# Kernel tuning notes

Hardware: AMD Instinct MI355X
Metric: run time of the kernel (lower is better)

The kernel has to match this reference:

```python
import jax, jax.numpy as jnp
import numpy as np

FEATURE_SCALE = 0.25  # cfg.feature_scale
G = 4                 # deformable/offset groups
K = 3                 # deform kernel size
KK = K * K
PAD = 1


def conv2d(x, w, b=None):
    y = jax.lax.conv_general_dilated(x, w, (1, 1), ((PAD, PAD), (PAD, PAD)),
                                     dimension_numbers=('NCHW', 'OIHW', 'NCHW'))
    return y if b is None else y + b[None, :, None, None]


def bilinear_upsample_ac(x, fs):
    # F.interpolate(mode='bilinear', align_corners=True, scale_factor=fs)
    b, c, H, W = x.shape
    Ho, Wo = H * fs, W * fs
    sy = jnp.arange(Ho, dtype=x.dtype) * ((H - 1) / (Ho - 1))
    sx = jnp.arange(Wo, dtype=x.dtype) * ((W - 1) / (Wo - 1))
    y0 = jnp.clip(jnp.floor(sy).astype(jnp.int32), 0, H - 2)
    x0 = jnp.clip(jnp.floor(sx).astype(jnp.int32), 0, W - 2)
    wy = (sy - y0)[None, None, :, None]
    wx = (sx - x0)[None, None, None, :]
    rows = x[:, :, y0, :] * (1 - wy) + x[:, :, y0 + 1, :] * wy
    return rows[:, :, :, x0] * (1 - wx) + rows[:, :, :, x0 + 1] * wx


def deform_conv(x, offset, mask, w):
    # torchvision.ops.deform_conv2d, stride 1, pad 1, weight groups = 1,
    # offset/mask groups = G. offset layout: (b, G*KK*2, H, W), (dy, dx) pairs.
    b, C, H, W = x.shape
    Cg = C // G
    off = offset.reshape(b, G, KK, 2, H, W)
    ii = (jnp.arange(KK) // K).reshape(1, 1, KK, 1, 1).astype(x.dtype)
    jj = (jnp.arange(KK) % K).reshape(1, 1, KK, 1, 1).astype(x.dtype)
    ys = jnp.arange(H, dtype=x.dtype).reshape(1, 1, 1, H, 1)
    xs = jnp.arange(W, dtype=x.dtype).reshape(1, 1, 1, 1, W)
    py = ys - PAD + ii + off[:, :, :, 0]   # (b,G,KK,H,W)
    px = xs - PAD + jj + off[:, :, :, 1]
    xt = x.reshape(b, G, Cg, H, W).transpose(0, 1, 3, 4, 2)  # (b,G,H,W,Cg)
    y0f = jnp.floor(py)
    x0f = jnp.floor(px)
    wy = py - y0f
    wx = px - x0f
    y0 = y0f.astype(jnp.int32)
    x0 = x0f.astype(jnp.int32)
    bi = jnp.arange(b).reshape(b, 1, 1, 1, 1)
    gi = jnp.arange(G).reshape(1, G, 1, 1, 1)

    def corner(yi, xi, wgt):
        valid = ((yi >= 0) & (yi < H) & (xi >= 0) & (xi < W)).astype(x.dtype)
        v = xt[bi, gi, jnp.clip(yi, 0, H - 1), jnp.clip(xi, 0, W - 1)]  # (b,G,KK,H,W,Cg)
        return v * (wgt * valid)[..., None]

    s = (corner(y0, x0, (1 - wy) * (1 - wx)) + corner(y0, x0 + 1, (1 - wy) * wx)
         + corner(y0 + 1, x0, wy * (1 - wx)) + corner(y0 + 1, x0 + 1, wy * wx))
    s = s * mask.reshape(b, G, KK, H, W)[..., None]
    wr = w.reshape(w.shape[0], G, Cg, KK)
    return jnp.einsum('bgkhwc,ogck->bohw', s, wr)


def _align(sou_list, ref_list, params):
    cat_feat, offset_vs = [], []
    for i in (3, 2, 1):
        sou, ref = sou_list[i - 1], ref_list[i - 1]
        b, C, H, W = sou.shape
        Cg = C // G
        off_w, off_b, mod_w, mod_b, reg_w = params[i]
        off_in = jnp.concatenate([sou.reshape(b, G, Cg, H, W),
                                  ref.reshape(b, G, Cg, H, W)], axis=2)
        off_in = off_in.reshape(b * G, 2 * Cg, H, W)
        offset = conv2d(off_in, off_w, off_b).reshape(b, G * 2 * KK, H, W)
        rng = min(H, W) * 0.5 / 2
        offset_map = rng * 2 * jax.nn.sigmoid(offset) - rng
        modulator = 2.0 * jax.nn.sigmoid(conv2d(sou, mod_w, mod_b))
        feat = deform_conv(sou, offset_map, modulator, reg_w)
        fs = int(1 // (FEATURE_SCALE / 2 ** (i - 1)))
        oy = jnp.mean(offset_map[:, 0::2], axis=1, keepdims=True)
        ox = jnp.mean(offset_map[:, 1::2], axis=1, keepdims=True)
        ov = bilinear_upsample_ac(jnp.concatenate([oy, ox], axis=1), fs) * fs
        cat_feat.append(feat)
        offset_vs.append(ov)
    return tuple(cat_feat) + tuple(offset_vs)


def setup_inputs() -> dict:
    key = jax.random.key(0)
    ks = jax.random.split(key, 32)
    d = {}
    shapes = {1: (2, 64, 128, 128), 2: (2, 64, 64, 64), 3: (2, 64, 32, 32)}
    k = 0
    for i in (1, 2, 3):
        d[f'sou{i}'] = jax.random.normal(ks[k], shapes[i], jnp.float32); k += 1
        d[f'ref{i}'] = jax.random.normal(ks[k], shapes[i], jnp.float32); k += 1
    Cg = 64 // G
    for i in (1, 2, 3):
        d[f'off_w{i}'] = jax.random.normal(ks[k], (2 * KK, 2 * Cg, K, K), jnp.float32) * 0.05; k += 1
        d[f'off_b{i}'] = jax.random.normal(ks[k], (2 * KK,), jnp.float32) * 0.05; k += 1
        d[f'mod_w{i}'] = jax.random.normal(ks[k], (G * KK, 64, K, K), jnp.float32) * 0.05; k += 1
        d[f'mod_b{i}'] = jax.random.normal(ks[k], (G * KK,), jnp.float32) * 0.05; k += 1
        d[f'reg_w{i}'] = jax.random.normal(ks[k], (64, 64, K, K), jnp.float32) * 0.05; k += 1
    return d


def reference(sou1, sou2, sou3, ref1, ref2, ref3,
              off_w1, off_b1, mod_w1, mod_b1, reg_w1,
              off_w2, off_b2, mod_w2, mod_b2, reg_w2,
              off_w3, off_b3, mod_w3, mod_b3, reg_w3):
    params = {1: (off_w1, off_b1, mod_w1, mod_b1, reg_w1),
              2: (off_w2, off_b2, mod_w2, mod_b2, reg_w2),
              3: (off_w3, off_b3, mod_w3, mod_b3, reg_w3)}
    return _align([sou1, sou2, sou3], [ref1, ref2, ref3], params)
```

## Files before the change

kernel.cpp:

```cpp
#include <hip/hip_runtime.h>

typedef __attribute__((ext_vector_type(8))) short short8;
typedef __attribute__((ext_vector_type(4))) float f32x4;

__device__ __forceinline__ float sigmoidf_(float x) { return 1.f / (1.f + __expf(-x)); }
__device__ __forceinline__ unsigned bf16rne(float x) {
    unsigned b = __float_as_uint(x);
    return (b + 0x7FFFu + ((b >> 16) & 1u)) >> 16;
}


struct P {
    const float *sou0, *sou1, *sou2;
    const float *ref0, *ref1, *ref2;
    const float *ob0, *ob1, *ob2;
    const float *mb0, *mb1, *mb2;
    float* out;
    float* ws;
};

union U {
    uint4 u4; int4 i4; short8 s8; f32x4 f4;
};

__global__ __launch_bounds__(256) void repack_all(
    const float* __restrict__ ow0, const float* __restrict__ mw0, const float* __restrict__ rw0,
    const float* __restrict__ ow1, const float* __restrict__ mw1, const float* __restrict__ rw1,
    const float* __restrict__ ow2, const float* __restrict__ mw2, const float* __restrict__ rw2,
    float* __restrict__ dst) {
    const int lvl = blockIdx.y;
    const float* ow = lvl == 0 ? ow0 : (lvl == 1 ? ow1 : ow2);
    const float* mw = lvl == 0 ? mw0 : (lvl == 1 ? mw1 : mw2);
    const float* rw = lvl == 0 ? rw0 : (lvl == 1 ? rw1 : rw2);
    unsigned* d = (unsigned*)(dst + lvl * 62784);
    int i = blockIdx.x * 256 + threadIdx.x;
    if (i < 18432) {
        int jw = i & 3;
        int lane = (i >> 2) & 63;
        int t3 = i >> 8;
        int ks = t3 % 18, wvu = t3 / 18;
        int o = wvu * 16 + (lane & 15);
        int c0 = ks * 32 + (lane >> 4) * 8 + 2 * jw;
        int g0 = c0 / 144, r0 = c0 % 144;
        int c1 = c0 + 1;
        int g1 = c1 / 144, r1 = c1 % 144;
        float w0 = rw[o * 576 + (g0 * 16 + (r0 & 15)) * 9 + (r0 >> 4)];
        float w1 = rw[o * 576 + (g1 * 16 + (r1 & 15)) * 9 + (r1 >> 4)];
        d[i] = bf16rne(w0) | (bf16rne(w1) << 16);
    } else if (i < 23552) {
        int o2 = i - 18432;
        int jw = o2 & 3;
        int lane = (o2 >> 2) & 63;
        int t2 = o2 >> 8;
        int nt = t2 & 1;
        int hk = t2 >> 1;
        int ks = hk % 5, h = hk / 5;
        int n = nt * 16 + (lane & 15);
        int K = ks * 32 + (lane >> 4) * 8 + 2 * jw;
        int tap = K >> 4, ch = K & 15;
        bool ok = (n < 18) && (tap < 9);
        float w0 = ok ? ow[n * 288 + (h * 16 + ch) * 9 + tap] : 0.f;
        float w1 = ok ? ow[n * 288 + (h * 16 + ch + 1) * 9 + tap] : 0.f;
        d[36864 + o2] = bf16rne(w0) | (bf16rne(w1) << 16);
    } else if (i < 37376) {
        int o3 = i - 23552;
        int jw = o3 & 3;
        int lane = (o3 >> 2) & 63;
        int t3 = o3 >> 8;
        int nt = t3 % 3, tc = t3 / 3;
        int tap = tc >> 1, c = tc & 1;
        int n = nt * 16 + (lane & 15);
        int ic0 = c * 32 + (lane >> 4) * 8 + 2 * jw;
        float w0 = (n < 36) ? mw[n * 576 + ic0 * 9 + tap] : 0.f;
        float w1 = (n < 36) ? mw[n * 576 + (ic0 + 1) * 9 + tap] : 0.f;
        d[41984 + o3] = bf16rne(w0) | (bf16rne(w1) << 16);
    }
}

__global__ __launch_bounds__(256, 2) void k1_prep(P p) {
    __shared__ __align__(16) char smem[28512];
    const int t = blockIdx.x;
    float* ws = p.ws;
    const int tid = threadIdx.x;

    int lvl, j;
    if (t < 512) { lvl = 0; j = t; }
    else if (t < 640) { lvl = 1; j = t - 512; }
    else { lvl = 2; j = t - 640; }
    const int logW = 7 - lvl;
    const int W = 1 << logW, H = W, HW = H * W;
    const int nper = 256 >> (2 * lvl);
    const int qb = j % nper, b = j / nper;
    const int q0 = qb * 64;
    const int hlo = q0 >> logW;
    const int xlo = q0 & (W - 1);
    const int cols = (W >= 64) ? 66 : 34;
    const int rcTot = (W >= 64) ? 198 : 136;
    const float* sou = lvl == 0 ? p.sou0 : (lvl == 1 ? p.sou1 : p.sou2);
    const float* ref = lvl == 0 ? p.ref0 : (lvl == 1 ? p.ref1 : p.ref2);
    const float* base_s = sou + (size_t)b * 64 * HW;
    const float* base_r = ref + (size_t)b * 64 * HW;
    unsigned* ldsW = (unsigned*)smem;
    const bool sact = tid < rcTot;
    const int srow = tid / cols, scol = tid - srow * cols;
    const int grow = hlo - 1 + srow, gcol = xlo - 1 + scol;
    const bool inb = sact && grow >= 0 && grow < H && gcol >= 0 && gcol < W;
    const size_t goff = inb ? ((size_t)grow * W + gcol) : 0;

    float vs[64];
#pragma unroll
    for (int c8 = 0; c8 < 8; ++c8) {
        const float* p0 = base_s + (size_t)(c8 * 8) * HW;
#pragma unroll
        for (int jj = 0; jj < 8; ++jj)
            vs[c8 * 8 + jj] = inb ? p0[(size_t)jj * HW + goff] : 0.f;
    }
    if (sact) {
#pragma unroll
        for (int c8 = 0; c8 < 8; ++c8) {
            uint4 wv;
            wv.x = bf16rne(vs[c8 * 8 + 0]) | (bf16rne(vs[c8 * 8 + 1]) << 16);
            wv.y = bf16rne(vs[c8 * 8 + 2]) | (bf16rne(vs[c8 * 8 + 3]) << 16);
            wv.z = bf16rne(vs[c8 * 8 + 4]) | (bf16rne(vs[c8 * 8 + 5]) << 16);
            wv.w = bf16rne(vs[c8 * 8 + 6]) | (bf16rne(vs[c8 * 8 + 7]) << 16);
            *(uint4*)&ldsW[tid * 36 + c8 * 4] = wv;
        }
    }
    __syncthreads();

    unsigned* XTb = (unsigned*)(ws + 4919232) +
                    (lvl == 0 ? 0 : (lvl == 1 ? 1048576 : 1310720));
#pragma unroll
    for (int u = 0; u < 2; ++u) {
        const int idx = tid * 2 + u;
        const int px = idx >> 3, gh = idx & 7;
        const int g = gh >> 1, half = gh & 1;
        const int rc = ((px >> logW) + 1) * cols + (px & (W - 1)) + 1;
        uint4 vv = *(const uint4*)&ldsW[rc * 36 + g * 8 + half * 4];
        *(uint4*)(XTb + ((size_t)(b * 4 + g) * HW + q0 + px) * 8 + half * 4) = vv;
    }

    float vr[64];
#pragma unroll
    for (int c8 = 0; c8 < 8; ++c8) {
        const float* p0 = base_r + (size_t)(c8 * 8) * HW;
#pragma unroll
        for (int jj = 0; jj < 8; ++jj)
            vr[c8 * 8 + jj] = inb ? p0[(size_t)jj * HW + goff] : 0.f;
    }

    const int wvu = __builtin_amdgcn_readfirstlane(tid >> 6);
    const int lane = tid & 63, quad = lane >> 4, lo16 = lane & 15;
    const int qg = q0 + wvu * 16 + lo16;
    const int rowB = (qg >> logW) - hlo;
    const int colB = (qg & (W - 1)) - xlo;
    const unsigned short* ldsS = (const unsigned short*)smem;
    const unsigned* WREPu = (const unsigned*)(ws + 4730880 + lvl * 62784);
    const unsigned* WBO2 = WREPu + 36864;
    const unsigned* WBM = WREPu + 41984;

    f32x4 accM[3], accO[4][2];
#pragma unroll
    for (int nt = 0; nt < 3; ++nt) accM[nt] = (f32x4){0.f, 0.f, 0.f, 0.f};
#pragma unroll
    for (int g = 0; g < 4; ++g)
#pragma unroll
        for (int nt = 0; nt < 2; ++nt) accO[g][nt] = (f32x4){0.f, 0.f, 0.f, 0.f};

#pragma unroll
    for (int tap = 0; tap < 9; ++tap) {
        const int ky = tap / 3, kx = tap - ky * 3;
        const int rc = (rowB + ky) * cols + colB + kx;
#pragma unroll
        for (int c = 0; c < 2; ++c) {
            U au; au.s8 = *(const short8*)&ldsS[rc * 72 + c * 32 + quad * 8];
#pragma unroll
            for (int nt = 0; nt < 3; ++nt) {
                U bu;
                bu.u4 = *(const uint4*)(WBM + (((tap * 2 + c) * 3 + nt) * 64 + lane) * 4);
                accM[nt] = __builtin_amdgcn_mfma_f32_16x16x32_bf16(au.s8, bu.s8, accM[nt], 0, 0, 0);
            }
        }
    }
#pragma unroll
    for (int ks = 0; ks < 5; ++ks) {
        const int Kbase = ks * 32 + quad * 8;
        const int tap = min(Kbase >> 4, 8);
        const int ky = tap / 3, kx = tap - ky * 3;
        const int rc = (rowB + ky) * cols + colB + kx;
        const int choff = Kbase & 15;
        U bu0, bu1;
        bu0.u4 = *(const uint4*)(WBO2 + ((ks * 2 + 0) * 64 + lane) * 4);
        bu1.u4 = *(const uint4*)(WBO2 + ((ks * 2 + 1) * 64 + lane) * 4);
#pragma unroll
        for (int g = 0; g < 4; ++g) {
            U au; au.s8 = *(const short8*)&ldsS[rc * 72 + g * 16 + choff];
            accO[g][0] = __builtin_amdgcn_mfma_f32_16x16x32_bf16(au.s8, bu0.s8, accO[g][0], 0, 0, 0);
            accO[g][1] = __builtin_amdgcn_mfma_f32_16x16x32_bf16(au.s8, bu1.s8, accO[g][1], 0, 0, 0);
        }
    }
    __syncthreads();

    if (sact) {
#pragma unroll
        for (int c8 = 0; c8 < 8; ++c8) {
            uint4 wv;
            wv.x = bf16rne(vr[c8 * 8 + 0]) | (bf16rne(vr[c8 * 8 + 1]) << 16);
            wv.y = bf16rne(vr[c8 * 8 + 2]) | (bf16rne(vr[c8 * 8 + 3]) << 16);
            wv.z = bf16rne(vr[c8 * 8 + 4]) | (bf16rne(vr[c8 * 8 + 5]) << 16);
            wv.w = bf16rne(vr[c8 * 8 + 6]) | (bf16rne(vr[c8 * 8 + 7]) << 16);
            *(uint4*)&ldsW[tid * 36 + c8 * 4] = wv;
        }
    }
    __syncthreads();

#pragma unroll
    for (int ks = 0; ks < 5; ++ks) {
        const int Kbase = ks * 32 + quad * 8;
        const int tap = min(Kbase >> 4, 8);
        const int ky = tap / 3, kx = tap - ky * 3;
        const int rc = (rowB + ky) * cols + colB + kx;
        const int choff = Kbase & 15;
        U bu0, bu1;
        bu0.u4 = *(const uint4*)(WBO2 + (((5 + ks) * 2 + 0) * 64 + lane) * 4);
        bu1.u4 = *(const uint4*)(WBO2 + (((5 + ks) * 2 + 1) * 64 + lane) * 4);
#pragma unroll
        for (int g = 0; g < 4; ++g) {
            U au; au.s8 = *(const short8*)&ldsS[rc * 72 + g * 16 + choff];
            accO[g][0] = __builtin_amdgcn_mfma_f32_16x16x32_bf16(au.s8, bu0.s8, accO[g][0], 0, 0, 0);
            accO[g][1] = __builtin_amdgcn_mfma_f32_16x16x32_bf16(au.s8, bu1.s8, accO[g][1], 0, 0, 0);
        }
    }

    {
        const float* bias = lvl == 0 ? p.mb0 : (lvl == 1 ? p.mb1 : p.mb2);
        float* MOD = ws + (lvl == 0 ? 3096576 : (lvl == 1 ? 4276224 : 4571136));
#pragma unroll
        for (int nt = 0; nt < 3; ++nt) {
            const int o = nt * 16 + lo16;
            if (o < 36) {
                const float bb = bias[o];
                float* op = MOD + (size_t)(b * 36 + o) * HW + q0 + wvu * 16 + quad * 4;
                *(float4*)op = make_float4(2.f * sigmoidf_(accM[nt][0] + bb),
                                           2.f * sigmoidf_(accM[nt][1] + bb),
                                           2.f * sigmoidf_(accM[nt][2] + bb),
                                           2.f * sigmoidf_(accM[nt][3] + bb));
            }
        }
    }
    {
        const float* bias = lvl == 0 ? p.ob0 : (lvl == 1 ? p.ob1 : p.ob2);
        float* OFFM = ws + (lvl == 0 ? 0 : (lvl == 1 ? 2359296 : 2949120));
        const float rng = 0.25f * (float)H;
        float macc[4] = {0.f, 0.f, 0.f, 0.f};
#pragma unroll
        for (int g = 0; g < 4; ++g)
#pragma unroll
            for (int nt = 0; nt < 2; ++nt) {
                const int o = nt * 16 + lo16;
                if (o < 18) {
                    const float bb = bias[o];
                    float ovv[4];
#pragma unroll
                    for (int rg = 0; rg < 4; ++rg)
                        ovv[rg] = rng * (2.f * sigmoidf_(accO[g][nt][rg] + bb) - 1.f);
                    float* op = OFFM + (size_t)(b * 72 + g * 18 + o) * HW + q0 + wvu * 16 + quad * 4;
                    *(float4*)op = make_float4(ovv[0], ovv[1], ovv[2], ovv[3]);
#pragma unroll
                    for (int rg = 0; rg < 4; ++rg) macc[rg] += ovv[rg];
                }
            }
        const bool odd = (lo16 & 1) != 0;
        float my[4], mx[4];
#pragma unroll
        for (int rg = 0; rg < 4; ++rg) {
            my[rg] = odd ? 0.f : macc[rg];
            mx[rg] = odd ? macc[rg] : 0.f;
        }
#pragma unroll
        for (int m = 1; m < 16; m <<= 1) {
#pragma unroll
            for (int rg = 0; rg < 4; ++rg) {
                my[rg] += __shfl_xor(my[rg], m);
                mx[rg] += __shfl_xor(mx[rg], m);
            }
        }
        if (lo16 == 0) {
            float* MEAN = ws + (lvl == 0 ? 4644864 : (lvl == 1 ? 4710400 : 4726784));
            const int pxb = q0 + wvu * 16 + quad * 4;
            const float inv = 1.f / 36.f;
            *(float4*)(MEAN + (size_t)(b * 2) * HW + pxb) =
                make_float4(my[0] * inv, my[1] * inv, my[2] * inv, my[3] * inv);
            *(float4*)(MEAN + (size_t)(b * 2 + 1) * HW + pxb) =
                make_float4(mx[0] * inv, mx[1] * inv, mx[2] * inv, mx[3] * inv);
        }
    }
}

__global__ __launch_bounds__(256) void k2_fused(P p) {
    __shared__ __align__(16) unsigned lds[32 * 292];
    const int t = blockIdx.x;
    float* ws = p.ws;
    const int tid = threadIdx.x;
    if (t < 1344) {
        int lvl, j;
        if (t < 1024) { lvl = 0; j = t; }
        else if (t < 1280) { lvl = 1; j = t - 1024; }
        else { lvl = 2; j = t - 1280; }
        const int logW = 7 - lvl;
        const int W = 1 << logW, H = W, HW = H * W;
        const int nper = 512 >> (2 * lvl);
        const int qb = j % nper, b = j / nper;
        const int q0 = qb * 32;
        const float* OFFM = ws + (lvl == 0 ? 0 : (lvl == 1 ? 2359296 : 2949120));
        const float* MOD = ws + (lvl == 0 ? 3096576 : (lvl == 1 ? 4276224 : 4571136));
        const unsigned* XTb = (const unsigned*)(ws + 4919232) +
                              (lvl == 0 ? 0 : (lvl == 1 ? 1048576 : 1310720));
        const unsigned* WB = (const unsigned*)(ws + 4730880 + lvl * 62784);
        float* outp = p.out + (lvl == 0 ? 655360 : (lvl == 1 ? 131072 : 0));
        const int wvu = __builtin_amdgcn_readfirstlane(tid >> 6);
        const int lane = tid & 63, quad = lane >> 4, lo16 = lane & 15;

        float dyv[5], dxv[5], mmv[5];
#pragma unroll
        for (int it = 0; it < 5; ++it) {
            const int tsk = it * 256 + tid;
            if (tsk < 1152) {
                const int gk = tsk >> 5, px = tsk & 31;
                const int g = gk / 9, k = gk - g * 9;
                const int q = q0 + px;
                dyv[it] = OFFM[(size_t)(b * 72 + g * 18 + 2 * k) * HW + q];
                dxv[it] = OFFM[(size_t)(b * 72 + g * 18 + 2 * k + 1) * HW + q];
                mmv[it] = MOD[(size_t)(b * 36 + g * 9 + k) * HW + q];
            }
        }
#pragma unroll
        for (int it = 0; it < 5; ++it) {
            const int tsk = it * 256 + tid;
            if (tsk < 1152) {
                const int gk = tsk >> 5, px = tsk & 31;
                const int g = gk / 9, k = gk - g * 9;
                const int q = q0 + px;
                const int h = q >> logW, xp = q & (W - 1);
                const int ky = k / 3, kx = k - ky * 3;
                float py = (float)(h - 1 + ky) + dyv[it];
                float pxx = (float)(xp - 1 + kx) + dxv[it];
                float y0f = floorf(py), x0f = floorf(pxx);
                float wy = py - y0f, wx = pxx - x0f;
                int y0 = (int)y0f, x0 = (int)x0f;
                const unsigned* xg = XTb + (size_t)(b * 4 + g) * HW * 8;
                float s[16];
#pragma unroll
                for (int cc = 0; cc < 16; ++cc) s[cc] = 0.f;
#pragma unroll
                for (int cor = 0; cor < 4; ++cor) {
                    int yy = y0 + (cor >> 1), xx = x0 + (cor & 1);
                    float cw = ((cor >> 1) ? wy : 1.f - wy) * ((cor & 1) ? wx : 1.f - wx);
                    cw = (yy >= 0 && yy < H && xx >= 0 && xx < W) ? cw * mmv[it] : 0.f;
                    int yc = min(max(yy, 0), H - 1), xc = min(max(xx, 0), W - 1);
                    const uint4* cp = (const uint4*)(xg + (size_t)((yc << logW) + xc) * 8);
                    unsigned cbuf[8];
                    *(uint4*)&cbuf[0] = cp[0];
                    *(uint4*)&cbuf[4] = cp[1];
#pragma unroll
                    for (int pr = 0; pr < 8; ++pr) {
                        float lo = __uint_as_float(cbuf[pr] << 16);
                        float hi = __uint_as_float(cbuf[pr] & 0xFFFF0000u);
                        s[2 * pr] = fmaf(cw, lo, s[2 * pr]);
                        s[2 * pr + 1] = fmaf(cw, hi, s[2 * pr + 1]);
                    }
                }
                unsigned* dp = &lds[px * 292 + gk * 8];
                uint4 w0, w1;
                w0.x = bf16rne(s[0]) | (bf16rne(s[1]) << 16);
                w0.y = bf16rne(s[2]) | (bf16rne(s[3]) << 16);
                w0.z = bf16rne(s[4]) | (bf16rne(s[5]) << 16);
                w0.w = bf16rne(s[6]) | (bf16rne(s[7]) << 16);
                w1.x = bf16rne(s[8]) | (bf16rne(s[9]) << 16);
                w1.y = bf16rne(s[10]) | (bf16rne(s[11]) << 16);
                w1.z = bf16rne(s[12]) | (bf16rne(s[13]) << 16);
                w1.w = bf16rne(s[14]) | (bf16rne(s[15]) << 16);
                *(uint4*)dp = w0;
                *(uint4*)(dp + 4) = w1;
            }
        }
        __syncthreads();

        f32x4 acc[2];
        acc[0] = (f32x4){0.f, 0.f, 0.f, 0.f};
        acc[1] = (f32x4){0.f, 0.f, 0.f, 0.f};
#pragma unroll
        for (int ks = 0; ks < 18; ++ks) {
            U bu;
            bu.u4 = *(const uint4*)(WB + (((wvu * 18 + ks) * 64 + lane) << 2));
#pragma unroll
            for (int mt = 0; mt < 2; ++mt) {
                U au;
                au.u4 = *(const uint4*)&lds[(mt * 16 + lo16) * 292 + ks * 16 + quad * 4];
                acc[mt] = __builtin_amdgcn_mfma_f32_16x16x32_bf16(au.s8, bu.s8, acc[mt], 0, 0, 0);
            }
        }
        float* op = outp + (size_t)(b * 64 + wvu * 16 + lo16) * HW + q0;
#pragma unroll
        for (int mt = 0; mt < 2; ++mt)
            *(f32x4*)(op + mt * 16 + quad * 4) = acc[mt];
    } else {
        int flat = ((t - 1344) * 256 + tid) * 4;
        int lvl = flat >> 20;
        int r = flat & 1048575;
        int b = r >> 19, c = (r >> 18) & 1;
        int pix = r & 262143;
        int yo = pix >> 9, xo = pix & 511;
        const int H = 128 >> lvl, W = H;
        const float* MEAN = ws + (lvl == 0 ? 4644864 : (lvl == 1 ? 4710400 : 4726784));
        const float* m = MEAN + (size_t)(b * 2 + c) * H * W;
        float* o = p.out + (lvl == 0 ? 4849664 : (lvl == 1 ? 3801088 : 2752512)) +
                   ((size_t)(b * 2 + c) * 512 + yo) * 512 + xo;
        const float fs = (float)(4 << lvl);
        const float sc = (float)(H - 1) * (1.f / 511.f);
        float sy = yo * sc;
        int y0 = min((int)sy, H - 2);
        float wy = sy - (float)y0;
        float rr[4];
#pragma unroll
        for (int u = 0; u < 4; ++u) {
            float sx = (float)(xo + u) * sc;
            int x0 = min((int)sx, W - 2);
            float wx = sx - (float)x0;
            float v00 = m[y0 * W + x0], v01 = m[y0 * W + x0 + 1];
            float v10 = m[(y0 + 1) * W + x0], v11 = m[(y0 + 1) * W + x0 + 1];
            float r0 = v00 * (1.f - wy) + v10 * wy;
            float r1 = v01 * (1.f - wy) + v11 * wy;
            rr[u] = (r0 * (1.f - wx) + r1 * wx) * fs;
        }
        *(float4*)o = make_float4(rr[0], rr[1], rr[2], rr[3]);
    }
}

extern "C" void kernel_launch(void* const* d_in, const int* in_sizes, int n_in,
                              void* d_out, int out_size, void* d_ws, size_t ws_size,
                              hipStream_t stream) {
    const float* fin[21];
    for (int i = 0; i < 21; ++i) fin[i] = (const float*)d_in[i];
    P p;
    if (in_sizes[1] == in_sizes[0]) {
        p.sou0 = fin[0]; p.ref0 = fin[1];
        p.sou1 = fin[2]; p.ref1 = fin[3];
        p.sou2 = fin[4]; p.ref2 = fin[5];
    } else {
        p.sou0 = fin[0]; p.sou1 = fin[1]; p.sou2 = fin[2];
        p.ref0 = fin[3]; p.ref1 = fin[4]; p.ref2 = fin[5];
    }
    p.ob0 = fin[7]; p.mb0 = fin[9];
    p.ob1 = fin[12]; p.mb1 = fin[14];
    p.ob2 = fin[17]; p.mb2 = fin[19];
    p.out = (float*)d_out;
    p.ws = (float*)d_ws;

    repack_all<<<dim3(146, 3), 256, 0, stream>>>(
        fin[6], fin[8], fin[10], fin[11], fin[13], fin[15], fin[16], fin[18], fin[20],
        p.ws + 4730880);
    k1_prep<<<dim3(672), 256, 0, stream>>>(p);
    k2_fused<<<dim3(4416), 256, 0, stream>>>(p);
}
```

Baseline: 168.1 us.

## Double k1_prep block to 512 threads and split mod/offset convs across waves

k1_prep now runs 512 threads per block. Each half of the threads loads 32 of the 64 channels for the halo tile, and waves 0-3 compute the modulation conv while waves 4-7 compute the offset conv, including the ref-feature pass. The ref load is hoisted before the XT transpose store so it overlaps the LDS phase. The aim is to cut per-thread register pressure and serial MFMA chain length and to raise memory-level parallelism, at the cost of more LDS contention per block and fewer resident blocks if occupancy limits bind.

```diff
diff --git a/kernel.cpp b/kernel.cpp
--- a/kernel.cpp
+++ b/kernel.cpp
@@ -77,7 +77,7 @@
     }
 }
 
-__global__ __launch_bounds__(256, 2) void k1_prep(P p) {
+__global__ __launch_bounds__(512, 4) void k1_prep(P p) {
     __shared__ __align__(16) char smem[28512];
     const int t = blockIdx.x;
     float* ws = p.ws;
@@ -101,57 +101,59 @@
     const float* base_s = sou + (size_t)b * 64 * HW;
     const float* base_r = ref + (size_t)b * 64 * HW;
     unsigned* ldsW = (unsigned*)smem;
-    const bool sact = tid < rcTot;
-    const int srow = tid / cols, scol = tid - srow * cols;
+
+    const int rc0 = tid & 255, chh = tid >> 8;
+    const bool sact = rc0 < rcTot;
+    const int srow = rc0 / cols, scol = rc0 - srow * cols;
     const int grow = hlo - 1 + srow, gcol = xlo - 1 + scol;
     const bool inb = sact && grow >= 0 && grow < H && gcol >= 0 && gcol < W;
     const size_t goff = inb ? ((size_t)grow * W + gcol) : 0;
 
-    float vs[64];
-#pragma unroll
-    for (int c8 = 0; c8 < 8; ++c8) {
-        const float* p0 = base_s + (size_t)(c8 * 8) * HW;
+    float vs[32];
+#pragma unroll
+    for (int c8 = 0; c8 < 4; ++c8) {
+        const float* p0 = base_s + (size_t)(chh * 32 + c8 * 8) * HW;
 #pragma unroll
         for (int jj = 0; jj < 8; ++jj)
             vs[c8 * 8 + jj] = inb ? p0[(size_t)jj * HW + goff] : 0.f;
     }
     if (sact) {
 #pragma unroll
-        for (int c8 = 0; c8 < 8; ++c8) {
+        for (int c8 = 0; c8 < 4; ++c8) {
             uint4 wv;
             wv.x = bf16rne(vs[c8 * 8 + 0]) | (bf16rne(vs[c8 * 8 + 1]) << 16);
             wv.y = bf16rne(vs[c8 * 8 + 2]) | (bf16rne(vs[c8 * 8 + 3]) << 16);
             wv.z = bf16rne(vs[c8 * 8 + 4]) | (bf16rne(vs[c8 * 8 + 5]) << 16);
             wv.w = bf16rne(vs[c8 * 8 + 6]) | (bf16rne(vs[c8 * 8 + 7]) << 16);
-            *(uint4*)&ldsW[tid * 36 + c8 * 4] = wv;
+            *(uint4*)&ldsW[rc0 * 36 + chh * 16 + c8 * 4] = wv;
         }
     }
     __syncthreads();
+
+    float vr[32];
+#pragma unroll
+    for (int c8 = 0; c8 < 4; ++c8) {
+        const float* p0 = base_r + (size_t)(chh * 32 + c8 * 8) * HW;
+#pragma unroll
+        for (int jj = 0; jj < 8; ++jj)
+            vr[c8 * 8 + jj] = inb ? p0[(size_t)jj * HW + goff] : 0.f;
+    }
 
     unsigned* XTb = (unsigned*)(ws + 4919232) +
                     (lvl == 0 ? 0 : (lvl == 1 ? 1048576 : 1310720));
-#pragma unroll
-    for (int u = 0; u < 2; ++u) {
-        const int idx = tid * 2 + u;
+    {
+        const int idx = tid;
         const int px = idx >> 3, gh = idx & 7;
         const int g = gh >> 1, half = gh & 1;
-        const int rc = ((px >> logW) + 1) * cols + (px & (W - 1)) + 1;
-        uint4 vv = *(const uint4*)&ldsW[rc * 36 + g * 8 + half * 4];
+        const int rcx = ((px >> logW) + 1) * cols + (px & (W - 1)) + 1;
+        uint4 vv = *(const uint4*)&ldsW[rcx * 36 + g * 8 + half * 4];
         *(uint4*)(XTb + ((size_t)(b * 4 + g) * HW + q0 + px) * 8 + half * 4) = vv;
-    }
-
-    float vr[64];
-#pragma unroll
-    for (int c8 = 0; c8 < 8; ++c8) {
-        const float* p0 = base_r + (size_t)(c8 * 8) * HW;
-#pragma unroll
-        for (int jj = 0; jj < 8; ++jj)
-            vr[c8 * 8 + jj] = inb ? p0[(size_t)jj * HW + goff] : 0.f;
     }
 
     const int wvu = __builtin_amdgcn_readfirstlane(tid >> 6);
     const int lane = tid & 63, quad = lane >> 4, lo16 = lane & 15;
-    const int qg = q0 + wvu * 16 + lo16;
+    const int qq = wvu & 3;
+    const int qg = q0 + qq * 16 + lo16;
     const int rowB = (qg >> logW) - hlo;
     const int colB = (qg & (W - 1)) - xlo;
     const unsigned short* ldsS = (const unsigned short*)smem;
@@ -167,72 +169,60 @@
 #pragma unroll
         for (int nt = 0; nt < 2; ++nt) accO[g][nt] = (f32x4){0.f, 0.f, 0.f, 0.f};
 
-#pragma unroll
-    for (int tap = 0; tap < 9; ++tap) {
-        const int ky = tap / 3, kx = tap - ky * 3;
-        const int rc = (rowB + ky) * cols + colB + kx;
-#pragma unroll
-        for (int c = 0; c < 2; ++c) {
-            U au; au.s8 = *(const short8*)&ldsS[rc * 72 + c * 32 + quad * 8];
-#pragma unroll
-            for (int nt = 0; nt < 3; ++nt) {
-                U bu;
-                bu.u4 = *(const uint4*)(WBM + (((tap * 2 + c) * 3 + nt) * 64 + lane) * 4);
-                accM[nt] = __builtin_amdgcn_mfma_f32_16x16x32_bf16(au.s8, bu.s8, accM[nt], 0, 0, 0);
-            }
-        }
-    }
-#pragma unroll
-    for (int ks = 0; ks < 5; ++ks) {
-        const int Kbase = ks * 32 + quad * 8;
-        const int tap = min(Kbase >> 4, 8);
-        const int ky = tap / 3, kx = tap - ky * 3;
-        const int rc = (rowB + ky) * cols + colB + kx;
-        const int choff = Kbase & 15;
-        U bu0, bu1;
-        bu0.u4 = *(const uint4*)(WBO2 + ((ks * 2 + 0) * 64 + lane) * 4);
-        bu1.u4 = *(const uint4*)(WBO2 + ((ks * 2 + 1) * 64 + lane) * 4);
-#pragma unroll
-        for (int g = 0; g < 4; ++g) {
-            U au; au.s8 = *(const short8*)&ldsS[rc * 72 + g * 16 + choff];
-            accO[g][0] = __builtin_amdgcn_mfma_f32_16x16x32_bf16(au.s8, bu0.s8, accO[g][0], 0, 0, 0);
-            accO[g][1] = __builtin_amdgcn_mfma_f32_16x16x32_bf16(au.s8, bu1.s8, accO[g][1], 0, 0, 0);
+    if (wvu < 4) {
+#pragma unroll
+        for (int tap = 0; tap < 9; ++tap) {
+            const int ky = tap / 3, kx = tap - ky * 3;
+            const int rcx = (rowB + ky) * cols + colB + kx;
+#pragma unroll
+            for (int c = 0; c < 2; ++c) {
+                U au; au.s8 = *(const short8*)&ldsS[rcx * 72 + c * 32 + quad * 8];
+#pragma unroll
+                for (int nt = 0; nt < 3; ++nt) {
+                    U bu;
+                    bu.u4 = *(const uint4*)(WBM + (((tap * 2 + c) * 3 + nt) * 64 + lane) * 4);
+                    accM[nt] =
+                        __builtin_amdgcn_mfma_f32_16x16x32_bf16(au.s8, bu.s8, accM[nt], 0, 0, 0);
+                }
+            }
+        }
+    } else {
+#pragma unroll
+        for (int ks = 0; ks < 5; ++ks) {
+            const int Kbase = ks * 32 + quad * 8;
+            const int tap = min(Kbase >> 4, 8);
+            const int ky = tap / 3, kx = tap - ky * 3;
+            const int rcx = (rowB + ky) * cols + colB + kx;
+            const int choff = Kbase & 15;
+            U bu0, bu1;
+            bu0.u4 = *(const uint4*)(WBO2 + ((ks * 2 + 0) * 64 + lane) * 4);
+            bu1.u4 = *(const uint4*)(WBO2 + ((ks * 2 + 1) * 64 + lane) * 4);
+#pragma unroll
+            for (int g = 0; g < 4; ++g) {
+                U au; au.s8 = *(const short8*)&ldsS[rcx * 72 + g * 16 + choff];
+                accO[g][0] =
+                    __builtin_amdgcn_mfma_f32_16x16x32_bf16(au.s8, bu0.s8, accO[g][0], 0, 0, 0);
+                accO[g][1] =
+                    __builtin_amdgcn_mfma_f32_16x16x32_bf16(au.s8, bu1.s8, accO[g][1], 0, 0, 0);
+            }
         }
     }
     __syncthreads();
 
     if (sact) {
 #pragma unroll
-        for (int c8 = 0; c8 < 8; ++c8) {
+        for (int c8 = 0; c8 < 4; ++c8) {
             uint4 wv;
             wv.x = bf16rne(vr[c8 * 8 + 0]) | (bf16rne(vr[c8 * 8 + 1]) << 16);
             wv.y = bf16rne(vr[c8 * 8 + 2]) | (bf16rne(vr[c8 * 8 + 3]) << 16);
             wv.z = bf16rne(vr[c8 * 8 + 4]) | (bf16rne(vr[c8 * 8 + 5]) << 16);
             wv.w = bf16rne(vr[c8 * 8 + 6]) | (bf16rne(vr[c8 * 8 + 7]) << 16);
-            *(uint4*)&ldsW[tid * 36 + c8 * 4] = wv;
+            *(uint4*)&ldsW[rc0 * 36 + chh * 16 + c8 * 4] = wv;
         }
     }
     __syncthreads();
 
-#pragma unroll
-    for (int ks = 0; ks < 5; ++ks) {
-        const int Kbase = ks * 32 + quad * 8;
-        const int tap = min(Kbase >> 4, 8);
-        const int ky = tap / 3, kx = tap - ky * 3;
-        const int rc = (rowB + ky) * cols + colB + kx;
-        const int choff = Kbase & 15;
-        U bu0, bu1;
-        bu0.u4 = *(const uint4*)(WBO2 + (((5 + ks) * 2 + 0) * 64 + lane) * 4);
-        bu1.u4 = *(const uint4*)(WBO2 + (((5 + ks) * 2 + 1) * 64 + lane) * 4);
-#pragma unroll
-        for (int g = 0; g < 4; ++g) {
-            U au; au.s8 = *(const short8*)&ldsS[rc * 72 + g * 16 + choff];
-            accO[g][0] = __builtin_amdgcn_mfma_f32_16x16x32_bf16(au.s8, bu0.s8, accO[g][0], 0, 0, 0);
-            accO[g][1] = __builtin_amdgcn_mfma_f32_16x16x32_bf16(au.s8, bu1.s8, accO[g][1], 0, 0, 0);
-        }
-    }
-
-    {
+    if (wvu < 4) {
         const float* bias = lvl == 0 ? p.mb0 : (lvl == 1 ? p.mb1 : p.mb2);
         float* MOD = ws + (lvl == 0 ? 3096576 : (lvl == 1 ? 4276224 : 4571136));
 #pragma unroll
@@ -240,15 +230,33 @@
             const int o = nt * 16 + lo16;
             if (o < 36) {
                 const float bb = bias[o];
-                float* op = MOD + (size_t)(b * 36 + o) * HW + q0 + wvu * 16 + quad * 4;
+                float* op = MOD + (size_t)(b * 36 + o) * HW + q0 + qq * 16 + quad * 4;
                 *(float4*)op = make_float4(2.f * sigmoidf_(accM[nt][0] + bb),
                                            2.f * sigmoidf_(accM[nt][1] + bb),
                                            2.f * sigmoidf_(accM[nt][2] + bb),
                                            2.f * sigmoidf_(accM[nt][3] + bb));
             }
         }
-    }
-    {
+    } else {
+#pragma unroll
+        for (int ks = 0; ks < 5; ++ks) {
+            const int Kbase = ks * 32 + quad * 8;
+            const int tap = min(Kbase >> 4, 8);
+            const int ky = tap / 3, kx = tap - ky * 3;
+            const int rcx = (rowB + ky) * cols + colB + kx;
+            const int choff = Kbase & 15;
+            U bu0, bu1;
+            bu0.u4 = *(const uint4*)(WBO2 + (((5 + ks) * 2 + 0) * 64 + lane) * 4);
+            bu1.u4 = *(const uint4*)(WBO2 + (((5 + ks) * 2 + 1) * 64 + lane) * 4);
+#pragma unroll
+            for (int g = 0; g < 4; ++g) {
+                U au; au.s8 = *(const short8*)&ldsS[rcx * 72 + g * 16 + choff];
+                accO[g][0] =
+                    __builtin_amdgcn_mfma_f32_16x16x32_bf16(au.s8, bu0.s8, accO[g][0], 0, 0, 0);
+                accO[g][1] =
+                    __builtin_amdgcn_mfma_f32_16x16x32_bf16(au.s8, bu1.s8, accO[g][1], 0, 0, 0);
+            }
+        }
         const float* bias = lvl == 0 ? p.ob0 : (lvl == 1 ? p.ob1 : p.ob2);
         float* OFFM = ws + (lvl == 0 ? 0 : (lvl == 1 ? 2359296 : 2949120));
         const float rng = 0.25f * (float)H;
@@ -264,7 +272,7 @@
 #pragma unroll
                     for (int rg = 0; rg < 4; ++rg)
                         ovv[rg] = rng * (2.f * sigmoidf_(accO[g][nt][rg] + bb) - 1.f);
-                    float* op = OFFM + (size_t)(b * 72 + g * 18 + o) * HW + q0 + wvu * 16 + quad * 4;
+                    float* op = OFFM + (size_t)(b * 72 + g * 18 + o) * HW + q0 + qq * 16 + quad * 4;
                     *(float4*)op = make_float4(ovv[0], ovv[1], ovv[2], ovv[3]);
 #pragma unroll
                     for (int rg = 0; rg < 4; ++rg) macc[rg] += ovv[rg];
@@ -287,7 +295,7 @@
         }
         if (lo16 == 0) {
             float* MEAN = ws + (lvl == 0 ? 4644864 : (lvl == 1 ? 4710400 : 4726784));
-            const int pxb = q0 + wvu * 16 + quad * 4;
+            const int pxb = q0 + qq * 16 + quad * 4;
             const float inv = 1.f / 36.f;
             *(float4*)(MEAN + (size_t)(b * 2) * HW + pxb) =
                 make_float4(my[0] * inv, my[1] * inv, my[2] * inv, my[3] * inv);
@@ -460,6 +468,6 @@
     repack_all<<<dim3(146, 3), 256, 0, stream>>>(
         fin[6], fin[8], fin[10], fin[11], fin[13], fin[15], fin[16], fin[18], fin[20],
         p.ws + 4730880);
-    k1_prep<<<dim3(672), 256, 0, stream>>>(p);
+    k1_prep<<<dim3(672), 512, 0, stream>>>(p);
     k2_fused<<<dim3(4416), 256, 0, stream>>>(p);
 }
```

Result: slower. 172.9 us (+2.8%).
